# Kernel optimization log

Hardware: AMD Instinct MI355X
Metric: run time of the kernel (lower is better)

## Reference

```python
import math
import jax, jax.numpy as jnp
import numpy as np

N_HEAD = 16
ROPE_BASE = 10000.0


def _rope_sin_cos(T, head_size, dtype):
    half = head_size // 2
    pos = jnp.arange(T, dtype=jnp.float32)[:, None]                      # [T,1]
    div = jnp.exp(jnp.arange(0, head_size, 2, dtype=jnp.float32) * (-math.log(ROPE_BASE) / head_size))  # [half]
    ang = pos * div                                                       # [T,half]
    return jnp.sin(ang).astype(dtype), jnp.cos(ang).astype(dtype)


def _apply_rope(q, k, sin, cos):
    # q,k: [B,T,H,D]; sin,cos: [T,D/2] -> broadcast [1,T,1,D/2]
    half = q.shape[-1] // 2
    sin = sin[None, :, None, :]
    cos = cos[None, :, None, :]
    q1, q2 = q[..., :half], q[..., half:]
    k1, k2 = k[..., :half], k[..., half:]
    q_rot = jnp.concatenate([q1 * cos - q2 * sin, q2 * cos + q1 * sin], axis=-1)
    k_rot = jnp.concatenate([k1 * cos - k2 * sin, k2 * cos + k1 * sin], axis=-1)
    return q_rot, k_rot


def setup_inputs() -> dict:
    key = jax.random.key(0)
    k1, k2, k3 = jax.random.split(key, 3)
    B, T, C = 2, 2048, 2048
    x = jax.random.normal(k1, (B, T, C), dtype=jnp.float32)
    qkv_w = jax.random.normal(k2, (3 * C, C), dtype=jnp.float32) * 0.02
    out_w = jax.random.normal(k3, (C, C), dtype=jnp.float32) * 0.02
    return {"x": x, "qkv_w": qkv_w, "out_w": out_w}


def reference(x, qkv_w, out_w):
    B, T, C = x.shape
    H = N_HEAD
    D = C // H
    qkv = (x @ qkv_w.T).reshape(B, T, 3, H, D)
    q, k, v = qkv[:, :, 0], qkv[:, :, 1], qkv[:, :, 2]   # [B,T,H,D]
    sin, cos = _rope_sin_cos(T, D, x.dtype)
    q, k = _apply_rope(q, k, sin, cos)
    scale = 1.0 / math.sqrt(D)
    scores = jnp.einsum('bthd,bshd->bhts', q, k) * scale  # [B,H,T,T]
    causal = jnp.tril(jnp.ones((T, T), dtype=bool))
    scores = jnp.where(causal[None, None], scores, jnp.finfo(scores.dtype).min)
    probs = jax.nn.softmax(scores, axis=-1)
    attn = jnp.einsum('bhts,bshd->bthd', probs, v)        # [B,T,H,D] (flash output layout)
    # Faithful to original: view(B,T,H,D).permute(0,2,1,3).reshape(B,T,C)
    attn = jnp.transpose(attn, (0, 2, 1, 3)).reshape(B, T, C)
    return attn @ out_w.T
```

## Files before the change

kernel.cpp:

```cpp
#include <hip/hip_runtime.h>

typedef __attribute__((ext_vector_type(8))) short short8;
typedef __attribute__((ext_vector_type(4))) float f32x4;

#define GLOAD16(g, l) __builtin_amdgcn_global_load_lds(                         \
    (const __attribute__((address_space(1))) void*)(g),                          \
    (__attribute__((address_space(3))) void*)(l), 16, 0, 0)

__device__ __forceinline__ float bf2f(unsigned short u) {
  union { unsigned int i; float f; } c; c.i = ((unsigned int)u) << 16; return c.f;
}
__device__ __forceinline__ unsigned short f2bf(float f) {
  union { float f; unsigned int i; } c; c.f = f;
  unsigned int u = c.i;
  u = (u + 0x7fffu + ((u >> 16) & 1u)) >> 16;
  return (unsigned short)u;
}

__global__ __launch_bounds__(256) void cvt_f32_bf16(const float* __restrict__ src,
                                                    unsigned short* __restrict__ dst,
                                                    int n8) {
  int i = blockIdx.x * 256 + threadIdx.x;
  if (i >= n8) return;
  const float4* s4 = (const float4*)src + (long)i * 2;
  float4 a = s4[0], b = s4[1];
  short8 o;
  o[0] = (short)f2bf(a.x); o[1] = (short)f2bf(a.y);
  o[2] = (short)f2bf(a.z); o[3] = (short)f2bf(a.w);
  o[4] = (short)f2bf(b.x); o[5] = (short)f2bf(b.y);
  o[6] = (short)f2bf(b.z); o[7] = (short)f2bf(b.w);
  *((short8*)dst + i) = o;
}

template<int OUT_F32>
__global__ __launch_bounds__(256) void gemm_bt(const unsigned short* __restrict__ A,
                                               const unsigned short* __restrict__ B,
                                               void* __restrict__ Cout,
                                               int M, int N, int K) {
  __shared__ __attribute__((aligned(16))) unsigned short Ah[128 * 64];
  __shared__ __attribute__((aligned(16))) unsigned short Bh[128 * 64];
  const int tid = threadIdx.x;
  const int l = tid & 63;
  const int w = tid >> 6;
  const int wm = w >> 1, wn = w & 1;
  const long brow = (long)blockIdx.y * 128;
  const long bcol = (long)blockIdx.x * 128;

  f32x4 acc[4][4];
#pragma unroll
  for (int i = 0; i < 4; ++i)
#pragma unroll
    for (int j = 0; j < 4; ++j) acc[i][j] = (f32x4){0.f, 0.f, 0.f, 0.f};

  const int srow = tid >> 3;
  const int sg = tid & 7;
  const int lwb = w << 10;

  for (int k0 = 0; k0 < K; k0 += 64) {
    __syncthreads();
#pragma unroll
    for (int i = 0; i < 4; ++i) {
      const int r = srow + i * 32;
      const int gp = (sg ^ (r & 7)) * 8;
      GLOAD16(A + (brow + r) * K + k0 + gp, (char*)Ah + lwb + i * 4096);
      GLOAD16(B + (bcol + r) * K + k0 + gp, (char*)Bh + lwb + i * 4096);
    }
    __syncthreads();
#pragma unroll
    for (int ks = 0; ks < 2; ++ks) {
      short8 af[4], bf[4];
#pragma unroll
      for (int mi = 0; mi < 4; ++mi) {
        const int row = wm * 64 + mi * 16 + (l & 15);
        const int byt = (row * 128 + (l >> 4) * 16 + ks * 64) ^ ((row & 7) << 4);
        af[mi] = *(const short8*)((const char*)Ah + byt);
      }
#pragma unroll
      for (int nj = 0; nj < 4; ++nj) {
        const int row = wn * 64 + nj * 16 + (l & 15);
        const int byt = (row * 128 + (l >> 4) * 16 + ks * 64) ^ ((row & 7) << 4);
        bf[nj] = *(const short8*)((const char*)Bh + byt);
      }
#pragma unroll
      for (int mi = 0; mi < 4; ++mi)
#pragma unroll
        for (int nj = 0; nj < 4; ++nj)
          acc[mi][nj] = __builtin_amdgcn_mfma_f32_16x16x32_bf16(af[mi], bf[nj],
                                                                acc[mi][nj], 0, 0, 0);
    }
  }

  const long rb = brow + wm * 64 + (l >> 4) * 4;
  const long cb = bcol + wn * 64 + (l & 15);
#pragma unroll
  for (int mi = 0; mi < 4; ++mi)
#pragma unroll
    for (int nj = 0; nj < 4; ++nj)
#pragma unroll
      for (int j = 0; j < 4; ++j) {
        const long row = rb + mi * 16 + j;
        const long col = cb + nj * 16;
        if (OUT_F32) ((float*)Cout)[row * N + col] = acc[mi][nj][j];
        else ((unsigned short*)Cout)[row * N + col] = f2bf(acc[mi][nj][j]);
      }
}

__global__ __launch_bounds__(256) void sincos_tab(float* __restrict__ tab) {
  int gid = blockIdx.x * 256 + threadIdx.x;
  int t = gid >> 6, d = gid & 63;
  float inv = expf(-(float)(2 * d) * 0.07195578415606394f);
  float ang = (float)t * inv;
  tab[2 * gid]     = sinf(ang);
  tab[2 * gid + 1] = cosf(ang);
}

__global__ __launch_bounds__(256) void rope_qk(unsigned short* __restrict__ qkv,
                                               const float* __restrict__ tab) {
  int gid = blockIdx.x * 256 + threadIdx.x;
  int m = gid >> 7;
  int h = (gid >> 3) & 15;
  int db = gid & 7;
  int t = m & 2047;
  long base = (long)m * 6144 + h * 128 + db * 8;
  const float* tp = tab + ((long)(t << 6) + db * 8) * 2;
  float4 t0 = *(const float4*)(tp + 0);
  float4 t1 = *(const float4*)(tp + 4);
  float4 t2 = *(const float4*)(tp + 8);
  float4 t3 = *(const float4*)(tp + 12);
  float sj[8] = {t0.x, t0.z, t1.x, t1.z, t2.x, t2.z, t3.x, t3.z};
  float cj[8] = {t0.y, t0.w, t1.y, t1.w, t2.y, t2.w, t3.y, t3.w};

  unsigned short* qp = qkv + base;
  short8 q1 = *(short8*)qp, q2 = *(short8*)(qp + 64);
  short8 o1, o2;
#pragma unroll
  for (int j = 0; j < 8; ++j) {
    float a = bf2f((unsigned short)q1[j]), bq = bf2f((unsigned short)q2[j]);
    o1[j] = (short)f2bf(a * cj[j] - bq * sj[j]);
    o2[j] = (short)f2bf(bq * cj[j] + a * sj[j]);
  }
  *(short8*)qp = o1; *(short8*)(qp + 64) = o2;

  unsigned short* kp = qkv + base + 2048;
  short8 k1 = *(short8*)kp, k2 = *(short8*)(kp + 64);
#pragma unroll
  for (int j = 0; j < 8; ++j) {
    float a = bf2f((unsigned short)k1[j]), bk = bf2f((unsigned short)k2[j]);
    o1[j] = (short)f2bf(a * cj[j] - bk * sj[j]);
    o2[j] = (short)f2bf(bk * cj[j] + a * sj[j]);
  }
  *(short8*)kp = o1; *(short8*)(kp + 64) = o2;
}

__global__ __launch_bounds__(256) void transpose_v(const unsigned short* __restrict__ qkv,
                                                   unsigned short* __restrict__ vt) {
  __shared__ __attribute__((aligned(16))) unsigned short tile[32][136];
  int tid = threadIdx.x;
  int t0 = blockIdx.x * 32;
  int bh = blockIdx.y;
  int b = bh >> 4, h = bh & 15;
  {
    int tt = tid >> 3;
    int dcb = (tid & 7) * 16;
    const unsigned short* src = qkv + (long)(b * 2048 + t0 + tt) * 6144 + 4096 + h * 128 + dcb;
    *(short8*)&tile[tt][dcb]     = *(const short8*)src;
    *(short8*)&tile[tt][dcb + 8] = *(const short8*)(src + 8);
  }
  __syncthreads();
  {
    int d = tid >> 1;
    int ts = (tid & 1) * 16;
    short8 o0, o1;
#pragma unroll
    for (int i = 0; i < 8; ++i) o0[i] = (short)tile[ts + i][d];
#pragma unroll
    for (int i = 0; i < 8; ++i) o1[i] = (short)tile[ts + 8 + i][d];
    unsigned short* dst = vt + (long)bh * 262144 + (long)d * 2048 + t0 + ts;
    *(short8*)dst       = o0;
    *(short8*)(dst + 8) = o1;
  }
}

#define STAGE(IT, BUF) do {                                                     \
    const int kv0s_ = (IT) * 64;                                                \
    _Pragma("unroll")                                                           \
    for (int i_ = 0; i_ < 4; ++i_) {                                            \
      const int kr_ = (tid >> 4) + i_ * 16;                                     \
      const int kgp_ = ((tid & 15) ^ (kr_ & 7)) * 8;                            \
      GLOAD16(qkv + (long)(b * 2048 + kv0s_ + kr_) * 6144 + 2048 + h * 128 + kgp_, \
              (char*)&Kh[BUF][0] + (w << 10) + i_ * 4096);                      \
      const int vr_ = (tid >> 3) + i_ * 32;                                     \
      const int vgp_ = ((tid & 7) ^ (vr_ & 7)) * 8;                             \
      GLOAD16(vt + (long)bh * 262144 + (long)vr_ * 2048 + kv0s_ + vgp_,         \
              (char*)&Vh[BUF][0] + (w << 10) + i_ * 4096);                      \
    }                                                                           \
  } while (0)

#define COMPUTE_TILE(QF, ACC, MR, LR, Q0, PHP, BUFB) do {                       \
    f32x4 s_[4];                                                                \
    _Pragma("unroll")                                                           \
    for (int kvt_ = 0; kvt_ < 4; ++kvt_) {                                      \
      s_[kvt_] = (f32x4){0.f, 0.f, 0.f, 0.f};                                   \
      _Pragma("unroll")                                                         \
      for (int dc_ = 0; dc_ < 4; ++dc_) {                                       \
        const int krow_ = kvt_ * 16 + (l & 15);                                 \
        const int byt_ = ((krow_ * 256 + (l >> 4) * 16 + dc_ * 64)              \
                          ^ ((krow_ & 7) << 4)) + (BUFB);                       \
        short8 kf_ = *(const short8*)((const char*)Kh + byt_);                  \
        s_[kvt_] = __builtin_amdgcn_mfma_f32_16x16x32_bf16(QF[dc_], kf_,        \
                                                           s_[kvt_], 0, 0, 0);  \
      }                                                                         \
    }                                                                           \
    const int qrc_ = (Q0) + w * 16 + ((l >> 4) << 2);                           \
    float mx_[4];                                                               \
    _Pragma("unroll") for (int j_ = 0; j_ < 4; ++j_) mx_[j_] = -1e30f;          \
    _Pragma("unroll")                                                           \
    for (int kvt_ = 0; kvt_ < 4; ++kvt_) {                                      \
      const int kvcol_ = kv0 + kvt_ * 16 + (l & 15);                            \
      _Pragma("unroll")                                                         \
      for (int j_ = 0; j_ < 4; ++j_) {                                          \
        float sv_ = s_[kvt_][j_];                                               \
        if (kvcol_ > qrc_ + j_) sv_ = -1e30f;                                   \
        s_[kvt_][j_] = sv_;                                                     \
        mx_[j_] = fmaxf(mx_[j_], sv_);                                          \
      }                                                                         \
    }                                                                           \
    float alpha_[4];                                                            \
    _Pragma("unroll")                                                           \
    for (int j_ = 0; j_ < 4; ++j_) {                                            \
      float v_ = mx_[j_];                                                       \
      v_ = fmaxf(v_, __shfl_xor(v_, 1));                                        \
      v_ = fmaxf(v_, __shfl_xor(v_, 2));                                        \
      v_ = fmaxf(v_, __shfl_xor(v_, 4));                                        \
      v_ = fmaxf(v_, __shfl_xor(v_, 8));                                        \
      float mnew_ = fmaxf((MR)[j_], v_);                                        \
      alpha_[j_] = exp2f((MR)[j_] - mnew_);                                     \
      (MR)[j_] = mnew_;                                                         \
    }                                                                           \
    float ps_[4] = {0.f, 0.f, 0.f, 0.f};                                        \
    _Pragma("unroll")                                                           \
    for (int kvt_ = 0; kvt_ < 4; ++kvt_) {                                      \
      _Pragma("unroll")                                                         \
      for (int j_ = 0; j_ < 4; ++j_) {                                          \
        float p_ = exp2f(s_[kvt_][j_] - (MR)[j_]);                              \
        ps_[j_] += p_;                                                          \
        const int prow_ = ((l >> 4) << 2) + j_;                                 \
        const int pcol_ = kvt_ * 16 + (l & 15);                                 \
        const int pb_ = (prow_ * 128 + pcol_ * 2) ^ ((prow_ & 7) << 4);         \
        *(unsigned short*)((char*)(PHP) + pb_) = f2bf(p_);                      \
      }                                                                         \
    }                                                                           \
    _Pragma("unroll")                                                           \
    for (int j_ = 0; j_ < 4; ++j_) {                                            \
      float v_ = ps_[j_];                                                       \
      v_ += __shfl_xor(v_, 1);                                                  \
      v_ += __shfl_xor(v_, 2);                                                  \
      v_ += __shfl_xor(v_, 4);                                                  \
      v_ += __shfl_xor(v_, 8);                                                  \
      (LR)[j_] = (LR)[j_] * alpha_[j_] + v_;                                    \
    }                                                                           \
    asm volatile("s_waitcnt lgkmcnt(0)" ::: "memory");                          \
    __builtin_amdgcn_sched_barrier(0);                                          \
    _Pragma("unroll")                                                           \
    for (int dn_ = 0; dn_ < 8; ++dn_)                                           \
      _Pragma("unroll")                                                         \
      for (int j_ = 0; j_ < 4; ++j_) (ACC)[dn_][j_] *= alpha_[j_];              \
    _Pragma("unroll")                                                           \
    for (int half_ = 0; half_ < 2; ++half_) {                                   \
      const int prw_ = (l & 15);                                                \
      const int pb_ = (prw_ * 128 + (l >> 4) * 16 + half_ * 64)                 \
                      ^ ((prw_ & 7) << 4);                                      \
      short8 pf_ = *(const short8*)((const char*)(PHP) + pb_);                  \
      _Pragma("unroll")                                                         \
      for (int dn_ = 0; dn_ < 8; ++dn_) {                                       \
        const int vrow_ = dn_ * 16 + (l & 15);                                  \
        const int vb_ = ((vrow_ * 128 + (l >> 4) * 16 + half_ * 64)             \
                         ^ ((vrow_ & 7) << 4)) + (BUFB);                        \
        short8 vf_ = *(const short8*)((const char*)Vh + vb_);                   \
        (ACC)[dn_] = __builtin_amdgcn_mfma_f32_16x16x32_bf16(pf_, vf_,          \
                                                             (ACC)[dn_], 0, 0, 0); \
      }                                                                         \
    }                                                                           \
  } while (0)

__global__ __launch_bounds__(256, 2) void flash_attn(const unsigned short* __restrict__ qkv,
                                                     const unsigned short* __restrict__ vt,
                                                     unsigned short* __restrict__ attn) {
  __shared__ __attribute__((aligned(16))) unsigned short Kh[2][64 * 128];
  __shared__ __attribute__((aligned(16))) unsigned short Vh[2][128 * 64];
  __shared__ __attribute__((aligned(16))) unsigned short Ph[4][2][16 * 64];

  const int tid = threadIdx.x;
  const int l = tid & 63;
  const int w = tid >> 6;
  const int bh = blockIdx.y;
  const int b = bh >> 4, h = bh & 15;
  const int qtA = blockIdx.x;
  const int qtB = 31 - qtA;
  const int q0A = qtA * 64, q0B = qtB * 64;
  const int endA = q0A + 64;
  const int nIter = qtB + 1;
  const float qscale = 0.08838834764831845f * 1.4426950408889634f;

  short8 qfA[4], qfB[4];
  {
    const int qrA = q0A + w * 16 + (l & 15);
    const int qrB = q0B + w * 16 + (l & 15);
    const unsigned short* qpA = qkv + (long)(b * 2048 + qrA) * 6144 + h * 128 + (l >> 4) * 8;
    const unsigned short* qpB = qkv + (long)(b * 2048 + qrB) * 6144 + h * 128 + (l >> 4) * 8;
#pragma unroll
    for (int dc = 0; dc < 4; ++dc) {
      short8 va = *(const short8*)(qpA + dc * 32);
      short8 vb = *(const short8*)(qpB + dc * 32);
#pragma unroll
      for (int j = 0; j < 8; ++j) {
        va[j] = (short)f2bf(bf2f((unsigned short)va[j]) * qscale);
        vb[j] = (short)f2bf(bf2f((unsigned short)vb[j]) * qscale);
      }
      qfA[dc] = va; qfB[dc] = vb;
    }
  }

  f32x4 accA[8], accB[8];
#pragma unroll
  for (int i = 0; i < 8; ++i) {
    accA[i] = (f32x4){0.f, 0.f, 0.f, 0.f};
    accB[i] = (f32x4){0.f, 0.f, 0.f, 0.f};
  }
  float mA[4], lA[4], mB[4], lB[4];
#pragma unroll
  for (int j = 0; j < 4; ++j) { mA[j] = -INFINITY; lA[j] = 0.f; mB[j] = -INFINITY; lB[j] = 0.f; }

  STAGE(0, 0);
  __syncthreads();
  for (int it = 0; it < nIter; ++it) {
    const int kv0 = it * 64;
    if (it + 1 < nIter) STAGE(it + 1, (it + 1) & 1);
    const int bufb = (it & 1) * 16384;
    COMPUTE_TILE(qfB, accB, mB, lB, q0B, (char*)&Ph[w][0][0], bufb);
    if (kv0 < endA) COMPUTE_TILE(qfA, accA, mA, lA, q0A, (char*)&Ph[w][1][0], bufb);
    __syncthreads();
  }

#pragma unroll
  for (int dn = 0; dn < 8; ++dn)
#pragma unroll
    for (int j = 0; j < 4; ++j) {
      const int qrowB = q0B + w * 16 + ((l >> 4) << 2) + j;
      const int qrowA = q0A + w * 16 + ((l >> 4) << 2) + j;
      const int d = dn * 16 + (l & 15);
      attn[((long)bh * 2048 + qrowB) * 128 + d] = f2bf(accB[dn][j] / lB[j]);
      attn[((long)bh * 2048 + qrowA) * 128 + d] = f2bf(accA[dn][j] / lA[j]);
    }
}

extern "C" void kernel_launch(void* const* d_in, const int* in_sizes, int n_in,
                              void* d_out, int out_size, void* d_ws, size_t ws_size,
                              hipStream_t stream) {
  (void)in_sizes; (void)n_in; (void)out_size; (void)ws_size;
  const float* x  = (const float*)d_in[0];
  const float* qw = (const float*)d_in[1];
  const float* ow = (const float*)d_in[2];
  float* out = (float*)d_out;
  char* ws = (char*)d_ws;

  unsigned short* xb    = (unsigned short*)(ws + 0);
  unsigned short* wqb   = (unsigned short*)(ws + 16777216);
  unsigned short* qkvb  = (unsigned short*)(ws + 41943040);
  float*          tabf  = (float*)(ws + 0);
  unsigned short* vtb   = (unsigned short*)(ws + 0);
  unsigned short* attnb = (unsigned short*)(ws + 16777216);
  unsigned short* wob   = (unsigned short*)(ws + 33554432);

  cvt_f32_bf16<<<4096, 256, 0, stream>>>(x, xb, 1048576);
  cvt_f32_bf16<<<6144, 256, 0, stream>>>(qw, wqb, 1572864);
  gemm_bt<0><<<dim3(48, 32), 256, 0, stream>>>(xb, wqb, (void*)qkvb, 4096, 6144, 2048);
  sincos_tab<<<512, 256, 0, stream>>>(tabf);
  cvt_f32_bf16<<<2048, 256, 0, stream>>>(ow, wob, 524288);
  rope_qk<<<2048, 256, 0, stream>>>(qkvb, tabf);
  transpose_v<<<dim3(64, 32), 256, 0, stream>>>(qkvb, vtb);
  flash_attn<<<dim3(16, 32), 256, 0, stream>>>(qkvb, vtb, attnb);
  gemm_bt<1><<<dim3(16, 32), 256, 0, stream>>>(attnb, wob, (void*)out, 4096, 2048, 2048);
}
```

Measured before the change: 428.7 us.

## Replace GEMM with triple-buffered 256x128-tile kernel and XCD-aware block swizzle

Replaces the single-buffered 128x128 bf16 GEMM with a 512-thread kernel using 256x128 output tiles and a three-stage LDS ring. Tiles are prefetched two steps ahead with direct global-to-LDS loads, and explicit vmcnt waits plus barriers overlap memory with MFMA work. Workgroup indices are remapped so neighbouring tiles spread across the 8 XCDs, aiming for better L2 reuse. Both the QKV and output projections use it; the cost is about 144KB of LDS per block, which limits each CU to one block.

```diff
diff --git a/kernel.cpp b/kernel.cpp
--- a/kernel.cpp
+++ b/kernel.cpp
@@ -33,39 +33,76 @@
 }
 
 template<int OUT_F32>
-__global__ __launch_bounds__(256) void gemm_bt(const unsigned short* __restrict__ A,
-                                               const unsigned short* __restrict__ B,
-                                               void* __restrict__ Cout,
-                                               int M, int N, int K) {
-  __shared__ __attribute__((aligned(16))) unsigned short Ah[128 * 64];
-  __shared__ __attribute__((aligned(16))) unsigned short Bh[128 * 64];
+__global__ __launch_bounds__(512, 1) void gemm_bt2(const unsigned short* __restrict__ A,
+                                                   const unsigned short* __restrict__ B,
+                                                   void* __restrict__ Cout,
+                                                   int M, int N, int K) {
+  __shared__ __attribute__((aligned(16))) unsigned short Ah[3][256 * 64];
+  __shared__ __attribute__((aligned(16))) unsigned short Bh[3][128 * 64];
+
   const int tid = threadIdx.x;
   const int l = tid & 63;
   const int w = tid >> 6;
-  const int wm = w >> 1, wn = w & 1;
-  const long brow = (long)blockIdx.y * 128;
-  const long bcol = (long)blockIdx.x * 128;
-
-  f32x4 acc[4][4];
-#pragma unroll
-  for (int i = 0; i < 4; ++i)
-#pragma unroll
-    for (int j = 0; j < 4; ++j) acc[i][j] = (f32x4){0.f, 0.f, 0.f, 0.f};
+  const int wm = w >> 1;
+  const int wn = w & 1;
+
+  const int nwg = gridDim.x * gridDim.y;
+  const int lin = blockIdx.y * gridDim.x + blockIdx.x;
+  const int cpx = nwg >> 3;
+  const int sw = (lin & 7) * cpx + (lin >> 3);
+  const int bx = sw % gridDim.x;
+  const int by = sw / gridDim.x;
+  const long brow = (long)by * 256;
+  const long bcol = (long)bx * 128;
 
   const int srow = tid >> 3;
   const int sg = tid & 7;
   const int lwb = w << 10;
 
-  for (int k0 = 0; k0 < K; k0 += 64) {
-    __syncthreads();
-#pragma unroll
-    for (int i = 0; i < 4; ++i) {
-      const int r = srow + i * 32;
-      const int gp = (sg ^ (r & 7)) * 8;
-      GLOAD16(A + (brow + r) * K + k0 + gp, (char*)Ah + lwb + i * 4096);
-      GLOAD16(B + (bcol + r) * K + k0 + gp, (char*)Bh + lwb + i * 4096);
+#define STAGE2(T) do {                                                          \
+    const int bufi_ = (T) % 3;                                                  \
+    const int k0_ = (T) * 64;                                                   \
+    _Pragma("unroll")                                                           \
+    for (int is_ = 0; is_ < 4; ++is_) {                                         \
+      const int r_ = is_ * 64 + srow;                                           \
+      const int gp_ = (sg ^ (r_ & 7)) * 8;                                      \
+      GLOAD16(A + (brow + r_) * K + k0_ + gp_,                                  \
+              (char*)&Ah[bufi_][0] + is_ * 8192 + lwb);                         \
+    }                                                                           \
+    _Pragma("unroll")                                                           \
+    for (int is_ = 0; is_ < 2; ++is_) {                                         \
+      const int r_ = is_ * 64 + srow;                                           \
+      const int gp_ = (sg ^ (r_ & 7)) * 8;                                      \
+      GLOAD16(B + (bcol + r_) * K + k0_ + gp_,                                  \
+              (char*)&Bh[bufi_][0] + is_ * 8192 + lwb);                         \
+    }                                                                           \
+  } while (0)
+
+  f32x4 acc[4][4];
+#pragma unroll
+  for (int i = 0; i < 4; ++i)
+#pragma unroll
+    for (int j = 0; j < 4; ++j) acc[i][j] = (f32x4){0.f, 0.f, 0.f, 0.f};
+
+  const int tlast = (K >> 6) - 1;
+  STAGE2(0);
+  STAGE2(1);
+
+  for (int t = 0; t <= tlast; ++t) {
+    if (t + 2 <= tlast) {
+      STAGE2(t + 2);
+      asm volatile("s_waitcnt vmcnt(12)" ::: "memory");
+    } else if (t + 1 <= tlast) {
+      asm volatile("s_waitcnt vmcnt(6)" ::: "memory");
+    } else {
+      asm volatile("s_waitcnt vmcnt(0)" ::: "memory");
     }
-    __syncthreads();
+    __builtin_amdgcn_sched_barrier(0);
+    __builtin_amdgcn_s_barrier();
+    __builtin_amdgcn_sched_barrier(0);
+
+    const char* Ab = (const char*)&Ah[t % 3][0];
+    const char* Bb = (const char*)&Bh[t % 3][0];
 #pragma unroll
     for (int ks = 0; ks < 2; ++ks) {
       short8 af[4], bf[4];
@@ -73,13 +110,13 @@
       for (int mi = 0; mi < 4; ++mi) {
         const int row = wm * 64 + mi * 16 + (l & 15);
         const int byt = (row * 128 + (l >> 4) * 16 + ks * 64) ^ ((row & 7) << 4);
-        af[mi] = *(const short8*)((const char*)Ah + byt);
+        af[mi] = *(const short8*)(Ab + byt);
       }
 #pragma unroll
       for (int nj = 0; nj < 4; ++nj) {
         const int row = wn * 64 + nj * 16 + (l & 15);
         const int byt = (row * 128 + (l >> 4) * 16 + ks * 64) ^ ((row & 7) << 4);
-        bf[nj] = *(const short8*)((const char*)Bh + byt);
+        bf[nj] = *(const short8*)(Bb + byt);
       }
 #pragma unroll
       for (int mi = 0; mi < 4; ++mi)
@@ -88,6 +125,8 @@
           acc[mi][nj] = __builtin_amdgcn_mfma_f32_16x16x32_bf16(af[mi], bf[nj],
                                                                 acc[mi][nj], 0, 0, 0);
     }
+    __builtin_amdgcn_sched_barrier(0);
+    __builtin_amdgcn_s_barrier();
   }
 
   const long rb = brow + wm * 64 + (l >> 4) * 4;
@@ -103,6 +142,7 @@
         if (OUT_F32) ((float*)Cout)[row * N + col] = acc[mi][nj][j];
         else ((unsigned short*)Cout)[row * N + col] = f2bf(acc[mi][nj][j]);
       }
+#undef STAGE2
 }
 
 __global__ __launch_bounds__(256) void sincos_tab(float* __restrict__ tab) {
@@ -181,6 +221,7 @@
   }
 }
 
+#define LOG2E 1.4426950408889634f
 #define STAGE(IT, BUF) do {                                                     \
     const int kv0s_ = (IT) * 64;                                                \
     _Pragma("unroll")                                                           \
@@ -374,11 +415,11 @@
 
   cvt_f32_bf16<<<4096, 256, 0, stream>>>(x, xb, 1048576);
   cvt_f32_bf16<<<6144, 256, 0, stream>>>(qw, wqb, 1572864);
-  gemm_bt<0><<<dim3(48, 32), 256, 0, stream>>>(xb, wqb, (void*)qkvb, 4096, 6144, 2048);
+  gemm_bt2<0><<<dim3(48, 16), 512, 0, stream>>>(xb, wqb, (void*)qkvb, 4096, 6144, 2048);
   sincos_tab<<<512, 256, 0, stream>>>(tabf);
   cvt_f32_bf16<<<2048, 256, 0, stream>>>(ow, wob, 524288);
   rope_qk<<<2048, 256, 0, stream>>>(qkvb, tabf);
   transpose_v<<<dim3(64, 32), 256, 0, stream>>>(qkvb, vtb);
   flash_attn<<<dim3(16, 32), 256, 0, stream>>>(qkvb, vtb, attnb);
-  gemm_bt<1><<<dim3(16, 32), 256, 0, stream>>>(attnb, wob, (void*)out, 4096, 2048, 2048);
-}
+  gemm_bt2<1><<<dim3(16, 16), 512, 0, stream>>>(attnb, wob, (void*)out, 4096, 2048, 2048);
+}
```

Result: slower. 441.1 us (+2.9%).
